# Kernel optimization log

Hardware: AMD Instinct MI355X
Metric: run time of the kernel (lower is better)

The kernel has to match this reference:

```python
import jax, jax.numpy as jnp
import numpy as np
from jax import lax

B, T_Y, T_X = 16, 1600, 400
MEL_C, TXT_C, MAS_C = 80, 512, 384
HID = MAS_C * 2          # SwiGLUConvFFN hidden width (mas_channels*2)
NEG = -1e9


def setup_inputs() -> dict:
    key = jax.random.key(0)
    ks = jax.random.split(key, 20)
    p = lambda k, s: jax.random.normal(k, s, jnp.float32) * 0.02
    return {
        "mel_hidden_states": jax.random.normal(ks[0], (B, T_Y, MEL_C), jnp.float32),
        "text_hidden_states": jax.random.normal(ks[1], (B, T_X, TXT_C), jnp.float32),
        # mel SwiGLU conv-FFN (kernel 5): in->2*HID, gate, HID->MAS_C
        "mel_w1": p(ks[2], (2 * HID, MEL_C, 5)), "mel_b1": jnp.zeros((2 * HID,), jnp.float32),
        "mel_w2": p(ks[3], (MAS_C, HID, 5)),     "mel_b2": jnp.zeros((MAS_C,), jnp.float32),
        # text SwiGLU conv-FFN (kernel 3)
        "txt_w1": p(ks[4], (2 * HID, TXT_C, 3)), "txt_b1": jnp.zeros((2 * HID,), jnp.float32),
        "txt_w2": p(ks[5], (MAS_C, HID, 3)),     "txt_b2": jnp.zeros((MAS_C,), jnp.float32),
        # SimpleAttention query/key projections (value proj does not affect returned outputs)
        "wq": p(ks[6], (MAS_C, MAS_C)), "bq": jnp.zeros((MAS_C,), jnp.float32),
        "wk": p(ks[7], (MAS_C, MAS_C)), "bk": jnp.zeros((MAS_C,), jnp.float32),
        "x_lens": jax.random.randint(ks[8], (B,), T_X // 2, T_X + 1).astype(jnp.int32),
        "y_lens": jax.random.randint(ks[9], (B,), T_Y // 2, T_Y + 1).astype(jnp.int32),
    }


def _conv_ffn(x, pad_mask, w1, b1, w2, b2):
    """SwiGLU/ReGLU conv FFN. x:(B,T,C), pad_mask:(B,T) True=padded."""
    keep = (~pad_mask)[:, None, :].astype(x.dtype)          # (B,1,T)
    h = jnp.transpose(x, (0, 2, 1)) * keep                  # (B,C,T)
    dn = ("NCH", "OIH", "NCH")
    h = lax.conv_general_dilated(h, w1, (1,), "SAME", dimension_numbers=dn) + b1[None, :, None]
    a, g = jnp.split(h, 2, axis=1)
    h = a * jax.nn.relu(g) * keep                           # relugt gating
    h = lax.conv_general_dilated(h, w2, (1,), "SAME", dimension_numbers=dn) + b2[None, :, None]
    return jnp.transpose(h * keep, (0, 2, 1))               # (B,T,out)


def _mas_single(logp, t_x, t_y):
    """Glow-TTS maximum_path for one item. logp:(T_X,T_Y). Returns hard path (T_X,T_Y)."""
    xi = jnp.arange(T_X)
    yi = jnp.arange(T_Y)
    valid = (xi[:, None] < t_x) & (yi[None, :] < t_y) & (xi[:, None] <= yi[None, :])
    lp = jnp.where(valid, logp, NEG)

    def fstep(prev, col):                                   # prev:(T_X,), col:(T_X,)
        shifted = jnp.concatenate([jnp.full((1,), NEG, prev.dtype), prev[:-1]])
        cur = col + jnp.maximum(prev, shifted)
        return cur, cur

    init = jnp.where(xi == 0, 0.0, NEG).astype(logp.dtype)
    _, v = lax.scan(fstep, init, lp.T)                      # v:(T_Y,T_X) DP table

    def bstep(x, y):                                        # backtrack from y=T_Y-1 down
        active = y < t_y
        row = (xi == x) & active
        vp = v[y - 1]
        dec = (x > 0) & ((x == y) | (vp[jnp.maximum(x - 1, 0)] > vp[x]))
        new_x = jnp.where(active & (y > 0) & dec, x - 1, x)
        return new_x, row

    _, rows = lax.scan(bstep, t_x - 1, jnp.arange(T_Y - 1, -1, -1))
    return rows[::-1].T.astype(jnp.float32)                 # (T_X,T_Y)


def _safe_log(t, eps=1e-6):
    return jnp.nan_to_num(jnp.log(t + eps), nan=eps)


def reference(mel_hidden_states, text_hidden_states,
              mel_w1, mel_b1, mel_w2, mel_b2,
              txt_w1, txt_b1, txt_w2, txt_b2,
              wq, bq, wk, bk, x_lens, y_lens):
    x_mask = jnp.arange(T_X)[None, :] >= x_lens[:, None]    # (B,T_X) True=padded
    y_mask = jnp.arange(T_Y)[None, :] >= y_lens[:, None]    # (B,T_Y)

    text_proj = _conv_ffn(text_hidden_states, x_mask, txt_w1, txt_b1, txt_w2, txt_b2)
    mel_proj = _conv_ffn(mel_hidden_states, y_mask, mel_w1, mel_b1, mel_w2, mel_b2)

    q = mel_proj @ wq.T + bq                                # (B,T_Y,D)
    k = text_proj @ wk.T + bk                               # (B,T_X,D)
    scores = jnp.einsum("byd,bxd->byx", q, k) / (MAS_C ** 0.5)
    # expand_masks: mask==0 only where query AND key are both padded (faithful to source)
    both_pad = y_mask[:, :, None] & x_mask[:, None, :]
    scores = jnp.where(both_pad, jnp.float32(-1e-9), scores)
    attn_w = jax.nn.softmax(scores, axis=-1)                # (B,T_Y,T_X)

    avg_attn = attn_w[:, None]                              # (B,1,T_Y,T_X)
    attn_logprob = _safe_log(avg_attn)

    mas_in = jnp.transpose(attn_logprob[:, 0], (0, 2, 1))   # (B,T_X,T_Y)
    attn_hard = lax.stop_gradient(jax.vmap(_mas_single)(mas_in, x_lens, y_lens))
    attn_hard_dur = attn_hard.sum(2)                        # (B,T_X)
    return avg_attn, attn_logprob, attn_hard, attn_hard_dur
```

## Files before the change

kernel.cpp:

```cpp
#include <hip/hip_runtime.h>
#include <cstdint>

#define B 16
#define TY 1600
#define TX 400
#define MAS 384
#define HID 768
#define NEGV -1e9f

typedef __bf16 bf16x8 __attribute__((ext_vector_type(8)));
typedef float  f32x4  __attribute__((ext_vector_type(4)));

__device__ __forceinline__ f32x4 mfma16(bf16x8 a, bf16x8 b, f32x4 c) {
  return __builtin_amdgcn_mfma_f32_16x16x32_bf16(a, b, c, 0, 0, 0);
}

__global__ void split_pad_k(const float* __restrict__ in, __bf16* __restrict__ oh,
                            __bf16* __restrict__ ol, int CIN, int CINP, long n) {
  long i = (long)blockIdx.x * 256 + threadIdx.x;
  if (i >= n) return;
  long row = i / CINP; int ci = (int)(i - row * CINP);
  float v = (ci < CIN) ? in[row * CIN + ci] : 0.f;
  __bf16 h = (__bf16)v;
  oh[i] = h; ol[i] = (__bf16)(v - (float)h);
}

__global__ void wsplit_k(const float* __restrict__ w, __bf16* __restrict__ oh,
                         __bf16* __restrict__ ol, int CIN, int K_, int CINP, long n) {
  long i = (long)blockIdx.x * 256 + threadIdx.x;
  if (i >= n) return;
  long kdspan = (long)K_ * CINP;
  long nn = i / kdspan; int kd = (int)(i - nn * kdspan);
  int k = kd / CINP, ci = kd - k * CINP;
  float v = (ci < CIN) ? w[(nn * CIN + ci) * K_ + k] : 0.f;
  __bf16 h = (__bf16)v;
  oh[i] = h; ol[i] = (__bf16)(v - (float)h);
}

template<int CINP, int K, int T>
__global__ __launch_bounds__(256)
void conv1_mfma(const __bf16* __restrict__ xh, const __bf16* __restrict__ xl,
                const __bf16* __restrict__ wh, const __bf16* __restrict__ wl,
                const float* __restrict__ bias, const int* __restrict__ lens,
                __bf16* __restrict__ hh, __bf16* __restrict__ hl)
{
  constexpr int BM = 128, PAD = K / 2, ROWS = BM + K - 1, KD = K * CINP;
  __shared__ float4 xs[8 * ROWS];
  const int b = blockIdx.z, t0 = blockIdx.x * BM, n0 = blockIdx.y * 64;
  const int tid = threadIdx.x, wid = tid >> 6, lane = tid & 63;
  const int wm = wid >> 1, wn = wid & 1, lr = lane & 15, lg = lane >> 4;
  const int len = lens[b];
  const f32x4 Z4 = {0.f, 0.f, 0.f, 0.f};
  f32x4 acc_a[4][2], acc_g[4][2];
  #pragma unroll
  for (int m = 0; m < 4; ++m)
    #pragma unroll
    for (int n = 0; n < 2; ++n) { acc_a[m][n] = Z4; acc_g[m][n] = Z4; }

  #pragma unroll 1
  for (int ci0 = 0; ci0 < CINP; ci0 += 32) {
    __syncthreads();
    for (int e = tid; e < ROWS * 8; e += 256) {
      int row = e >> 3, sc = e & 7, spl = sc >> 2, cg = sc & 3;
      int t = t0 + row - PAD;
      float4 v = {0.f, 0.f, 0.f, 0.f};
      if (t >= 0 && t < len)
        v = *(const float4*)((spl ? xl : xh) + ((size_t)b * T + t) * CINP + ci0 + cg * 8);
      xs[(spl * 4 + cg) * ROWS + row] = v;
    }
    __syncthreads();
    #pragma unroll
    for (int k = 0; k < K; ++k) {
      bf16x8 ah[4], al[4];
      #pragma unroll
      for (int mf = 0; mf < 4; ++mf) {
        int row = wm * 64 + mf * 16 + lr + k;
        ah[mf] = *(const bf16x8*)&xs[lg * ROWS + row];
        al[mf] = *(const bf16x8*)&xs[(4 + lg) * ROWS + row];
      }
      size_t kd = (size_t)k * CINP + ci0 + lg * 8;
      #pragma unroll
      for (int nf = 0; nf < 2; ++nf) {
        int na = n0 + wn * 32 + nf * 16 + lr;
        bf16x8 bah = *(const bf16x8*)(wh + (size_t)na * KD + kd);
        bf16x8 bal = *(const bf16x8*)(wl + (size_t)na * KD + kd);
        bf16x8 bgh = *(const bf16x8*)(wh + (size_t)(na + HID) * KD + kd);
        bf16x8 bgl = *(const bf16x8*)(wl + (size_t)(na + HID) * KD + kd);
        #pragma unroll
        for (int mf = 0; mf < 4; ++mf) {
          acc_a[mf][nf] = mfma16(ah[mf], bah, acc_a[mf][nf]);
          acc_a[mf][nf] = mfma16(ah[mf], bal, acc_a[mf][nf]);
          acc_a[mf][nf] = mfma16(al[mf], bah, acc_a[mf][nf]);
          acc_g[mf][nf] = mfma16(ah[mf], bgh, acc_g[mf][nf]);
          acc_g[mf][nf] = mfma16(ah[mf], bgl, acc_g[mf][nf]);
          acc_g[mf][nf] = mfma16(al[mf], bgh, acc_g[mf][nf]);
        }
      }
    }
  }
  #pragma unroll
  for (int nf = 0; nf < 2; ++nf) {
    int c = n0 + wn * 32 + nf * 16 + lr;
    float ba = bias[c], bg = bias[c + HID];
    #pragma unroll
    for (int mf = 0; mf < 4; ++mf) {
      #pragma unroll
      for (int r = 0; r < 4; ++r) {
        int t = t0 + wm * 64 + mf * 16 + lg * 4 + r;
        if (t < T) {
          float a = acc_a[mf][nf][r] + ba;
          float g = acc_g[mf][nf][r] + bg;
          float v = a * fmaxf(g, 0.f);
          __bf16 vh = (__bf16)v;
          size_t o = ((size_t)b * T + t) * HID + c;
          hh[o] = vh;
          hl[o] = (__bf16)(v - (float)vh);
        }
      }
    }
  }
}

template<int CINP, int K, int T, bool MASK, bool SPLITOUT, bool STORET>
__global__ __launch_bounds__(256)
void conv2_mfma(const __bf16* __restrict__ xh, const __bf16* __restrict__ xl,
                const __bf16* __restrict__ wh, const __bf16* __restrict__ wl,
                const float* __restrict__ bias, const int* __restrict__ lens,
                float* __restrict__ out, __bf16* __restrict__ oh, __bf16* __restrict__ ol)
{
  constexpr int BM = 64, PAD = K / 2, ROWS = BM + K - 1, STRIDE = ROWS + 1, KD = K * CINP;
  __shared__ float4 xs[8 * STRIDE];
  const int b = blockIdx.z, t0 = blockIdx.x * BM, n0 = blockIdx.y * 128;
  const int tid = threadIdx.x, wn = tid >> 6, lane = tid & 63;
  const int lr = lane & 15, lg = lane >> 4;
  const int len = lens[b];
  const f32x4 Z4 = {0.f, 0.f, 0.f, 0.f};
  f32x4 acc[4][2];
  #pragma unroll
  for (int m = 0; m < 4; ++m)
    #pragma unroll
    for (int n = 0; n < 2; ++n) acc[m][n] = Z4;

  #pragma unroll 1
  for (int ci0 = 0; ci0 < CINP; ci0 += 32) {
    __syncthreads();
    for (int e = tid; e < ROWS * 8; e += 256) {
      int row = e >> 3, sc = e & 7, spl = sc >> 2, cg = sc & 3;
      int t = t0 + row - PAD;
      float4 v = {0.f, 0.f, 0.f, 0.f};
      if (t >= 0 && t < len)
        v = *(const float4*)((spl ? xl : xh) + ((size_t)b * T + t) * CINP + ci0 + cg * 8);
      xs[(spl * 4 + cg) * STRIDE + row] = v;
    }
    __syncthreads();
    #pragma unroll
    for (int k = 0; k < K; ++k) {
      bf16x8 ah[4], al[4];
      #pragma unroll
      for (int mf = 0; mf < 4; ++mf) {
        int row = mf * 16 + lr + k;
        ah[mf] = *(const bf16x8*)&xs[lg * STRIDE + row];
        al[mf] = *(const bf16x8*)&xs[(4 + lg) * STRIDE + row];
      }
      size_t kd = (size_t)k * CINP + ci0 + lg * 8;
      #pragma unroll
      for (int nf = 0; nf < 2; ++nf) {
        int nc = n0 + wn * 32 + nf * 16 + lr;
        bf16x8 bh = *(const bf16x8*)(wh + (size_t)nc * KD + kd);
        bf16x8 bl = *(const bf16x8*)(wl + (size_t)nc * KD + kd);
        #pragma unroll
        for (int mf = 0; mf < 4; ++mf) {
          acc[mf][nf] = mfma16(ah[mf], bh, acc[mf][nf]);
          acc[mf][nf] = mfma16(ah[mf], bl, acc[mf][nf]);
          acc[mf][nf] = mfma16(al[mf], bh, acc[mf][nf]);
        }
      }
    }
  }
  #pragma unroll
  for (int nf = 0; nf < 2; ++nf) {
    int c = n0 + wn * 32 + nf * 16 + lr;
    float bb = bias[c];
    #pragma unroll
    for (int mf = 0; mf < 4; ++mf) {
      #pragma unroll
      for (int r = 0; r < 4; ++r) {
        int t = t0 + mf * 16 + lg * 4 + r;
        if (t < T) {
          float v = acc[mf][nf][r] + bb;
          if (MASK && t >= len) v = 0.f;
          if (SPLITOUT) {
            __bf16 vh = (__bf16)v;
            size_t o = ((size_t)b * T + t) * MAS + c;
            oh[o] = vh;
            ol[o] = (__bf16)(v - (float)vh);
          } else if (STORET) {
            out[((size_t)b * MAS + c) * T + t] = v;
          } else {
            out[((size_t)b * T + t) * MAS + c] = v;
          }
        }
      }
    }
  }
}

__global__ __launch_bounds__(512)
void scores_k(const float* __restrict__ q, const float* __restrict__ kT,
              const int* __restrict__ xl, const int* __restrict__ yl,
              float* __restrict__ oattn, float* __restrict__ ologp)
{
  __shared__ float qs[16 * 384];
  __shared__ float tmp[8];
  const int b = blockIdx.y, y0 = blockIdx.x * 16, tid = threadIdx.x;
  for (int e = tid; e < 16 * 384; e += 512)
    qs[e] = q[((size_t)b * TY + (y0 + e / 384)) * 384 + (e - (e / 384) * 384)];
  __syncthreads();
  float acc[16];
  #pragma unroll
  for (int i = 0; i < 16; ++i) acc[i] = 0.f;
  const int x = tid;
  if (x < TX) {
    const float* kb = kT + (size_t)b * MAS * TX + x;
    for (int d = 0; d < 384; d += 4) {
      float k0 = kb[(size_t)(d + 0) * TX], k1 = kb[(size_t)(d + 1) * TX];
      float k2 = kb[(size_t)(d + 2) * TX], k3 = kb[(size_t)(d + 3) * TX];
      #pragma unroll
      for (int yy = 0; yy < 16; ++yy) {
        float4 qv = *(const float4*)&qs[yy * 384 + d];
        acc[yy] = fmaf(qv.x, k0, fmaf(qv.y, k1, fmaf(qv.z, k2, fmaf(qv.w, k3, acc[yy]))));
      }
    }
  }
  const int xlen = xl[b], ylen = yl[b];
  const float scale = 0.05103103630798288f;
  const bool xpad = (x >= xlen);
  const int wv = tid >> 6, ln = tid & 63;
  #pragma unroll 1
  for (int yy = 0; yy < 16; ++yy) {
    int y = y0 + yy;
    float s = -3.0e38f;
    if (x < TX) {
      s = acc[yy] * scale;
      if (xpad && (y >= ylen)) s = -1e-9f;
    }
    float m = s;
    for (int off = 32; off; off >>= 1) m = fmaxf(m, __shfl_xor(m, off));
    if (ln == 0) tmp[wv] = m;
    __syncthreads();
    float mx = fmaxf(fmaxf(fmaxf(tmp[0], tmp[1]), fmaxf(tmp[2], tmp[3])),
                     fmaxf(fmaxf(tmp[4], tmp[5]), fmaxf(tmp[6], tmp[7])));
    __syncthreads();
    float e = (x < TX) ? expf(s - mx) : 0.f;
    float sm = e;
    for (int off = 32; off; off >>= 1) sm += __shfl_xor(sm, off);
    if (ln == 0) tmp[wv] = sm;
    __syncthreads();
    float tot = tmp[0] + tmp[1] + tmp[2] + tmp[3] + tmp[4] + tmp[5] + tmp[6] + tmp[7];
    __syncthreads();
    if (x < TX) {
      float w = e / tot;
      size_t o = ((size_t)b * TY + y) * TX + x;
      oattn[o] = w;
      ologp[o] = logf(w + 1e-6f);
    }
  }
}

#define MAS_LD(blkv, buf) do {                                           \
    int base_ = (blkv) * 4;                                              \
    _Pragma("unroll")                                                    \
    for (int d_ = 0; d_ < 4; ++d_) {                                     \
      int yr_ = base_ + d_; if (yr_ > TY - 1) yr_ = TY - 1;              \
      const float* r_ = lpb + (size_t)yr_ * TX;                          \
      buf[d_ * 3 + 0] = *(const float4*)(r_ + lb0);                      \
      buf[d_ * 3 + 1] = *(const float4*)(r_ + lb1);                      \
      buf[d_ * 3 + 2] = *(const float4*)(r_ + lb2);                      \
    } } while (0)

#define MAS_BLK(blkv, buf) do {                                          \
    float h0 = __shfl_up(w[8], 1),  h1 = __shfl_up(w[9], 1);             \
    float h2 = __shfl_up(w[10], 1), h3 = __shfl_up(w[11], 1);            \
    w[0] = lane ? h0 : NEGV; w[1] = lane ? h1 : NEGV;                    \
    w[2] = lane ? h2 : NEGV; w[3] = lane ? h3 : NEGV;                    \
    const int y0_ = (blkv) * 4;                                          \
    const bool ph1_ = (y0_ < TX);                                        \
    _Pragma("unroll")                                                    \
    for (int d_ = 0; d_ < 4; ++d_) {                                     \
      const int y_ = y0_ + d_;                                           \
      float lp[12];                                                      \
      _Pragma("unroll")                                                  \
      for (int k_ = 0; k_ < 3; ++k_) {                                   \
        float4 v_ = buf[d_ * 3 + k_];                                    \
        lp[k_*4+0] = v_.x + wxm[k_*4+0]; lp[k_*4+1] = v_.y + wxm[k_*4+1];\
        lp[k_*4+2] = v_.z + wxm[k_*4+2]; lp[k_*4+3] = v_.w + wxm[k_*4+3];\
      }                                                                  \
      if (ph1_) {                                                        \
        int c_ = y_ - p0;                                                \
        _Pragma("unroll")                                                \
        for (int i_ = 0; i_ < 12; ++i_) lp[i_] = (i_ <= c_) ? lp[i_] : NEGV; \
      }                                                                  \
      unsigned byte_ = 0;                                                \
      _Pragma("unroll")                                                  \
      for (int j_ = 0; j_ < 8; ++j_)                                     \
        byte_ |= (w[j_ + 3] > w[j_ + 4]) ? (1u << j_) : 0u;              \
      float nw[12];                                                      \
      nw[0] = lp[0] + w[0];                                              \
      _Pragma("unroll")                                                  \
      for (int i_ = 1; i_ < 12; ++i_) nw[i_] = lp[i_] + fmaxf(w[i_], w[i_ - 1]); \
      bb[(size_t)y_ * 64 + lane] = (unsigned char)byte_;                 \
      _Pragma("unroll")                                                  \
      for (int i_ = 0; i_ < 12; ++i_) w[i_] = nw[i_];                    \
    } } while (0)

__global__ __launch_bounds__(64)
void mas_fwd(const float* __restrict__ logprob, const int* __restrict__ xl,
             const int* __restrict__ yl, unsigned char* __restrict__ bits)
{
  const int b = blockIdx.x;
  const int lane = threadIdx.x;
  const int xlen = xl[b], ylen = yl[b];
  const float* lpb = logprob + (size_t)b * TY * TX;
  unsigned char* bb = bits + (size_t)b * TY * 64;
  const int p0 = lane * 8 - 4;
  int t;
  t = p0;     if (t < 0) t = 0; if (t > 396) t = 396; const int lb0 = t;
  t = p0 + 4; if (t < 0) t = 0; if (t > 396) t = 396; const int lb1 = t;
  t = p0 + 8; if (t < 0) t = 0; if (t > 396) t = 396; const int lb2 = t;

  float w[12], wxm[12];
  #pragma unroll
  for (int i = 0; i < 12; ++i) {
    int p = p0 + i;
    wxm[i] = (p >= 0 && p < xlen) ? 0.f : NEGV;
    w[i] = (p == 0) ? 0.f : NEGV;
  }

  float4 bufA[12], bufB[12];
  MAS_LD(0, bufA);
  MAS_LD(1, bufB);
  const int nblk = (ylen + 3) >> 2;
  int blk = 0;
  #pragma unroll 1
  for (; blk + 1 < nblk; blk += 2) {
    MAS_BLK(blk, bufA);
    MAS_LD(blk + 2, bufA);
    MAS_BLK(blk + 1, bufB);
    MAS_LD(blk + 3, bufB);
  }
  if (blk < nblk) MAS_BLK(blk, bufA);
}

__global__ __launch_bounds__(64)
void mas_bt(const unsigned char* __restrict__ bits, const int* __restrict__ xl,
            const int* __restrict__ yl, float* __restrict__ hard, float* __restrict__ dur)
{
  const int b = blockIdx.x;
  const int lane = threadIdx.x;
  const int xlen = xl[b], ylen = yl[b];
  const unsigned char* bb = bits + (size_t)b * TY * 64;
  float* hb = hard + (size_t)b * TX * TY;
  float* db = dur + (size_t)b * TX;

  int x = xlen - 1;
  int cnt = 0;
  #pragma unroll 1
  for (int ycur = ylen - 1; ycur >= 0; ycur -= 64) {
    int lo = x - 63; if (lo < 0) lo = 0;
    const int wb = (lo >> 3) & ~3;
    int ry = ycur - lane;
    unsigned w0 = 0, w1 = 0, w2 = 0;
    if (ry >= 0) {
      const unsigned* rp = (const unsigned*)(bb + (size_t)ry * 64 + wb);
      w0 = rp[0]; w1 = rp[1]; w2 = rp[2];
    }
    const int rows = (ycur + 1 < 64) ? (ycur + 1) : 64;
    #pragma unroll 1
    for (int s = 0; s < rows; s += 8) {
      const int cnt8 = (rows - s < 8) ? (rows - s) : 8;
      unsigned r0[8], r1[8], r2[8];
      #pragma unroll
      for (int u = 0; u < 8; ++u) {
        r0[u] = (unsigned)__builtin_amdgcn_readlane((int)w0, s + u);
        r1[u] = (unsigned)__builtin_amdgcn_readlane((int)w1, s + u);
        r2[u] = (unsigned)__builtin_amdgcn_readlane((int)w2, s + u);
      }
      #pragma unroll
      for (int u = 0; u < 8; ++u) {
        if (u < cnt8) {
          const int yy = ycur - s - u;
          ++cnt;
          if (yy > 0 && x > 0) {
            const int boff = (x >> 3) - wb;
            const unsigned word = (boff < 4) ? r0[u] : ((boff < 8) ? r1[u] : r2[u]);
            const unsigned byte = word >> ((boff & 3) * 8);
            if ((x == yy) || ((byte >> (x & 7)) & 1)) {
              for (int q = lane; q < cnt; q += 64) hb[(size_t)x * TY + yy + q] = 1.0f;
              if (lane == 0) db[x] = (float)cnt;
              cnt = 0;
              --x;
            }
          }
        }
      }
    }
  }
  for (int q = lane; q < cnt; q += 64) hb[(size_t)x * TY + q] = 1.0f;
  if (lane == 0) db[x] = (float)cnt;
}

extern "C" void kernel_launch(void* const* d_in, const int* in_sizes, int n_in,
                              void* d_out, int out_size, void* d_ws, size_t ws_size,
                              hipStream_t stream) {
  const float* mel_x  = (const float*)d_in[0];
  const float* txt_x  = (const float*)d_in[1];
  const float* mel_w1 = (const float*)d_in[2];
  const float* mel_b1 = (const float*)d_in[3];
  const float* mel_w2 = (const float*)d_in[4];
  const float* mel_b2 = (const float*)d_in[5];
  const float* txt_w1 = (const float*)d_in[6];
  const float* txt_b1 = (const float*)d_in[7];
  const float* txt_w2 = (const float*)d_in[8];
  const float* txt_b2 = (const float*)d_in[9];
  const float* wq     = (const float*)d_in[10];
  const float* bq     = (const float*)d_in[11];
  const float* wk     = (const float*)d_in[12];
  const float* bk     = (const float*)d_in[13];
  const int*   xl     = (const int*)d_in[14];
  const int*   yl     = (const int*)d_in[15];

  char* wsb = (char*)d_ws;
  constexpr size_t MXH  = 0;
  constexpr size_t MXL  = MXH  + 4915200;
  constexpr size_t TXH  = MXL  + 4915200;
  constexpr size_t TXL  = TXH  + 6553600;
  constexpr size_t TPH  = TXH;
  constexpr size_t TPL  = TXH  + 4915200;
  constexpr size_t W1MH = TXL  + 6553600;
  constexpr size_t W1ML = W1MH + 1474560;
  constexpr size_t W2MH = W1ML + 1474560;
  constexpr size_t W2ML = W2MH + 2949120;
  constexpr size_t W1TH = W2ML + 2949120;
  constexpr size_t W1TL = W1TH + 4718592;
  constexpr size_t W2TH = W1TL + 4718592;
  constexpr size_t W2TL = W2TH + 1769472;
  constexpr size_t WQH  = W2TL + 1769472;
  constexpr size_t WQL  = WQH  + 294912;
  constexpr size_t WKH  = WQL  + 294912;
  constexpr size_t WKL  = WKH  + 294912;
  constexpr size_t HH   = WKL  + 294912;
  constexpr size_t HL   = HH   + 39321600;
  constexpr size_t QB   = HH;
  constexpr size_t KTB  = HL;
  constexpr size_t BITS = HL   + 10240000;
  constexpr size_t PH   = HL   + 39321600;
  constexpr size_t PL   = PH   + 19660800;

  float* out = (float*)d_out;
  float* o_attn = out;
  float* o_logp = out + (size_t)10240000;
  float* o_hard = out + (size_t)20480000;
  float* o_dur  = out + (size_t)30720000;

  hipMemsetAsync(o_hard, 0, (size_t)(10240000 + 6400) * sizeof(float), stream);

  split_pad_k<<<9600, 256, 0, stream>>>(mel_x, (__bf16*)(wsb + MXH), (__bf16*)(wsb + MXL), 80, 96, 2457600L);
  split_pad_k<<<12800, 256, 0, stream>>>(txt_x, (__bf16*)(wsb + TXH), (__bf16*)(wsb + TXL), 512, 512, 3276800L);
  wsplit_k<<<2880, 256, 0, stream>>>(mel_w1, (__bf16*)(wsb + W1MH), (__bf16*)(wsb + W1ML), 80, 5, 96, 737280L);
  wsplit_k<<<5760, 256, 0, stream>>>(mel_w2, (__bf16*)(wsb + W2MH), (__bf16*)(wsb + W2ML), 768, 5, 768, 1474560L);
  wsplit_k<<<9216, 256, 0, stream>>>(txt_w1, (__bf16*)(wsb + W1TH), (__bf16*)(wsb + W1TL), 512, 3, 512, 2359296L);
  wsplit_k<<<3456, 256, 0, stream>>>(txt_w2, (__bf16*)(wsb + W2TH), (__bf16*)(wsb + W2TL), 768, 3, 768, 884736L);
  wsplit_k<<<576, 256, 0, stream>>>(wq, (__bf16*)(wsb + WQH), (__bf16*)(wsb + WQL), 384, 1, 384, 147456L);
  wsplit_k<<<576, 256, 0, stream>>>(wk, (__bf16*)(wsb + WKH), (__bf16*)(wsb + WKL), 384, 1, 384, 147456L);

  conv1_mfma<512, 3, 400><<<dim3(4, 12, B), 256, 0, stream>>>(
      (const __bf16*)(wsb + TXH), (const __bf16*)(wsb + TXL),
      (const __bf16*)(wsb + W1TH), (const __bf16*)(wsb + W1TL),
      txt_b1, xl, (__bf16*)(wsb + HH), (__bf16*)(wsb + HL));
  conv2_mfma<768, 3, 400, true, true, false><<<dim3(7, 3, B), 256, 0, stream>>>(
      (const __bf16*)(wsb + HH), (const __bf16*)(wsb + HL),
      (const __bf16*)(wsb + W2TH), (const __bf16*)(wsb + W2TL),
      txt_b2, xl, nullptr, (__bf16*)(wsb + TPH), (__bf16*)(wsb + TPL));

  conv1_mfma<96, 5, 1600><<<dim3(13, 12, B), 256, 0, stream>>>(
      (const __bf16*)(wsb + MXH), (const __bf16*)(wsb + MXL),
      (const __bf16*)(wsb + W1MH), (const __bf16*)(wsb + W1ML),
      mel_b1, yl, (__bf16*)(wsb + HH), (__bf16*)(wsb + HL));
  conv2_mfma<768, 5, 1600, true, true, false><<<dim3(25, 3, B), 256, 0, stream>>>(
      (const __bf16*)(wsb + HH), (const __bf16*)(wsb + HL),
      (const __bf16*)(wsb + W2MH), (const __bf16*)(wsb + W2ML),
      mel_b2, yl, nullptr, (__bf16*)(wsb + PH), (__bf16*)(wsb + PL));

  conv2_mfma<384, 1, 400, false, false, true><<<dim3(7, 3, B), 256, 0, stream>>>(
      (const __bf16*)(wsb + TPH), (const __bf16*)(wsb + TPL),
      (const __bf16*)(wsb + WKH), (const __bf16*)(wsb + WKL),
      bk, xl, (float*)(wsb + KTB), nullptr, nullptr);
  conv2_mfma<384, 1, 1600, false, false, false><<<dim3(25, 3, B), 256, 0, stream>>>(
      (const __bf16*)(wsb + PH), (const __bf16*)(wsb + PL),
      (const __bf16*)(wsb + WQH), (const __bf16*)(wsb + WQL),
      bq, yl, (float*)(wsb + QB), nullptr, nullptr);

  scores_k<<<dim3(100, B), 512, 0, stream>>>(
      (const float*)(wsb + QB), (const float*)(wsb + KTB), xl, yl, o_attn, o_logp);
  mas_fwd<<<B, 64, 0, stream>>>(o_logp, xl, yl, (unsigned char*)(wsb + BITS));
  mas_bt<<<B, 64, 0, stream>>>((const unsigned char*)(wsb + BITS), xl, yl, o_hard, o_dur);
}
```

Baseline: 1.639 ms.

## Fold Q/K projections into second conv weights and retile conv2

The Q and K linear projections are folded into the second conv-FFN convolution weights by precomputing Wq·W2 and Wk·W2 with an MFMA kernel, and the projected conv2 biases are folded into per-channel constants. This removes two projection GEMM launches and the bf16 split intermediate outputs of conv2. conv2 is also retiled to 512 threads covering 192 output channels per block. The fold adds a small per-call weight GEMM and changes rounding of the folded weights, though the hi/lo split keeps precision.

New measurement: 2.025 ms. 1.24x slower.

```diff
diff --git a/kernel.cpp b/kernel.cpp
--- a/kernel.cpp
+++ b/kernel.cpp
@@ -35,6 +35,90 @@
   float v = (ci < CIN) ? w[(nn * CIN + ci) * K_ + k] : 0.f;
   __bf16 h = (__bf16)v;
   oh[i] = h; ol[i] = (__bf16)(v - (float)h);
+}
+
+__global__ void tsplit_k(const float* __restrict__ in, __bf16* __restrict__ oh,
+                         __bf16* __restrict__ ol, int JTOT, long n) {
+  long i = (long)blockIdx.x * 256 + threadIdx.x;
+  if (i >= n) return;
+  int m = (int)(i / JTOT), j = (int)(i - (long)m * JTOT);
+  float v = in[i];
+  long o = (long)j * 384 + m;
+  __bf16 h = (__bf16)v;
+  oh[o] = h; ol[o] = (__bf16)(v - (float)h);
+}
+
+__global__ void fold_bias_k(const float* __restrict__ wq, const float* __restrict__ b,
+                            float* __restrict__ o) {
+  int n = threadIdx.x;
+  float s = 0.f;
+  for (int m = 0; m < 384; ++m) s = fmaf(wq[n * 384 + m], b[m], s);
+  o[n] = s;
+}
+
+template<int KK>
+__global__ __launch_bounds__(256)
+void fold_mfma(const __bf16* __restrict__ xh, const __bf16* __restrict__ xl,
+               const __bf16* __restrict__ wh, const __bf16* __restrict__ wl,
+               __bf16* __restrict__ oh, __bf16* __restrict__ ol)
+{
+  constexpr int CINP = 384, ROWS = 64, STRIDE = 65;
+  __shared__ float4 xs[8 * STRIDE];
+  const int t0 = blockIdx.x * 64, n0 = blockIdx.y * 128;
+  const int tid = threadIdx.x, wn = tid >> 6, lane = tid & 63;
+  const int lr = lane & 15, lg = lane >> 4;
+  const f32x4 Z4 = {0.f, 0.f, 0.f, 0.f};
+  f32x4 acc[4][2];
+  #pragma unroll
+  for (int m = 0; m < 4; ++m) { acc[m][0] = Z4; acc[m][1] = Z4; }
+
+  #pragma unroll 1
+  for (int ci0 = 0; ci0 < CINP; ci0 += 32) {
+    __syncthreads();
+    for (int e = tid; e < ROWS * 8; e += 256) {
+      int row = e >> 3, sc = e & 7, spl = sc >> 2, cg = sc & 3;
+      int t = t0 + row;
+      xs[(spl * 4 + cg) * STRIDE + row] =
+          *(const float4*)((spl ? xl : xh) + (size_t)t * CINP + ci0 + cg * 8);
+    }
+    __syncthreads();
+    bf16x8 ah[4], al[4];
+    #pragma unroll
+    for (int mf = 0; mf < 4; ++mf) {
+      int row = mf * 16 + lr;
+      ah[mf] = *(const bf16x8*)&xs[lg * STRIDE + row];
+      al[mf] = *(const bf16x8*)&xs[(4 + lg) * STRIDE + row];
+    }
+    size_t kd = (size_t)ci0 + lg * 8;
+    #pragma unroll
+    for (int nf = 0; nf < 2; ++nf) {
+      int nc = n0 + wn * 32 + nf * 16 + lr;
+      bf16x8 bh = *(const bf16x8*)(wh + (size_t)nc * 384 + kd);
+      bf16x8 bl = *(const bf16x8*)(wl + (size_t)nc * 384 + kd);
+      #pragma unroll
+      for (int mf = 0; mf < 4; ++mf) {
+        acc[mf][nf] = mfma16(ah[mf], bh, acc[mf][nf]);
+        acc[mf][nf] = mfma16(ah[mf], bl, acc[mf][nf]);
+        acc[mf][nf] = mfma16(al[mf], bh, acc[mf][nf]);
+      }
+    }
+  }
+  #pragma unroll
+  for (int nf = 0; nf < 2; ++nf) {
+    int c = n0 + wn * 32 + nf * 16 + lr;
+    #pragma unroll
+    for (int mf = 0; mf < 4; ++mf) {
+      #pragma unroll
+      for (int r = 0; r < 4; ++r) {
+        int j = t0 + mf * 16 + lg * 4 + r;
+        int k = j % KK, ci = j / KK;
+        size_t o = (size_t)c * (KK * HID) + (size_t)k * HID + ci;
+        float v = acc[mf][nf][r];
+        __bf16 vh = (__bf16)v;
+        oh[o] = vh; ol[o] = (__bf16)(v - (float)vh);
+      }
+    }
+  }
 }
 
 template<int CINP, int K, int T>
@@ -121,30 +205,30 @@
   }
 }
 
-template<int CINP, int K, int T, bool MASK, bool SPLITOUT, bool STORET>
-__global__ __launch_bounds__(256)
+template<int CINP, int K, int T, bool STORET>
+__global__ __launch_bounds__(512)
 void conv2_mfma(const __bf16* __restrict__ xh, const __bf16* __restrict__ xl,
                 const __bf16* __restrict__ wh, const __bf16* __restrict__ wl,
-                const float* __restrict__ bias, const int* __restrict__ lens,
-                float* __restrict__ out, __bf16* __restrict__ oh, __bf16* __restrict__ ol)
+                const float* __restrict__ bias, const float* __restrict__ ab,
+                const int* __restrict__ lens, float* __restrict__ out)
 {
   constexpr int BM = 64, PAD = K / 2, ROWS = BM + K - 1, STRIDE = ROWS + 1, KD = K * CINP;
   __shared__ float4 xs[8 * STRIDE];
-  const int b = blockIdx.z, t0 = blockIdx.x * BM, n0 = blockIdx.y * 128;
-  const int tid = threadIdx.x, wn = tid >> 6, lane = tid & 63;
-  const int lr = lane & 15, lg = lane >> 4;
+  const int b = blockIdx.z, t0 = blockIdx.x * BM, n0 = blockIdx.y * 192;
+  const int tid = threadIdx.x, wid = tid >> 6, lane = tid & 63;
+  const int wm = wid >> 2, wn = wid & 3, lr = lane & 15, lg = lane >> 4;
   const int len = lens[b];
   const f32x4 Z4 = {0.f, 0.f, 0.f, 0.f};
-  f32x4 acc[4][2];
-  #pragma unroll
-  for (int m = 0; m < 4; ++m)
-    #pragma unroll
-    for (int n = 0; n < 2; ++n) acc[m][n] = Z4;
+  f32x4 acc[2][3];
+  #pragma unroll
+  for (int m = 0; m < 2; ++m)
+    #pragma unroll
+    for (int n = 0; n < 3; ++n) acc[m][n] = Z4;
 
   #pragma unroll 1
   for (int ci0 = 0; ci0 < CINP; ci0 += 32) {
     __syncthreads();
-    for (int e = tid; e < ROWS * 8; e += 256) {
+    for (int e = tid; e < ROWS * 8; e += 512) {
       int row = e >> 3, sc = e & 7, spl = sc >> 2, cg = sc & 3;
       int t = t0 + row - PAD;
       float4 v = {0.f, 0.f, 0.f, 0.f};
@@ -155,21 +239,21 @@
     __syncthreads();
     #pragma unroll
     for (int k = 0; k < K; ++k) {
-      bf16x8 ah[4], al[4];
-      #pragma unroll
-      for (int mf = 0; mf < 4; ++mf) {
-        int row = mf * 16 + lr + k;
+      bf16x8 ah[2], al[2];
+      #pragma unroll
+      for (int mf = 0; mf < 2; ++mf) {
+        int row = wm * 32 + mf * 16 + lr + k;
         ah[mf] = *(const bf16x8*)&xs[lg * STRIDE + row];
         al[mf] = *(const bf16x8*)&xs[(4 + lg) * STRIDE + row];
       }
       size_t kd = (size_t)k * CINP + ci0 + lg * 8;
       #pragma unroll
-      for (int nf = 0; nf < 2; ++nf) {
-        int nc = n0 + wn * 32 + nf * 16 + lr;
+      for (int nf = 0; nf < 3; ++nf) {
+        int nc = n0 + wn * 48 + nf * 16 + lr;
         bf16x8 bh = *(const bf16x8*)(wh + (size_t)nc * KD + kd);
         bf16x8 bl = *(const bf16x8*)(wl + (size_t)nc * KD + kd);
         #pragma unroll
-        for (int mf = 0; mf < 4; ++mf) {
+        for (int mf = 0; mf < 2; ++mf) {
           acc[mf][nf] = mfma16(ah[mf], bh, acc[mf][nf]);
           acc[mf][nf] = mfma16(ah[mf], bl, acc[mf][nf]);
           acc[mf][nf] = mfma16(al[mf], bh, acc[mf][nf]);
@@ -178,27 +262,20 @@
     }
   }
   #pragma unroll
-  for (int nf = 0; nf < 2; ++nf) {
-    int c = n0 + wn * 32 + nf * 16 + lr;
-    float bb = bias[c];
-    #pragma unroll
-    for (int mf = 0; mf < 4; ++mf) {
+  for (int nf = 0; nf < 3; ++nf) {
+    int c = n0 + wn * 48 + nf * 16 + lr;
+    float bb = bias[c], aB = ab[c];
+    #pragma unroll
+    for (int mf = 0; mf < 2; ++mf) {
       #pragma unroll
       for (int r = 0; r < 4; ++r) {
-        int t = t0 + mf * 16 + lg * 4 + r;
+        int t = t0 + wm * 32 + mf * 16 + lg * 4 + r;
         if (t < T) {
           float v = acc[mf][nf][r] + bb;
-          if (MASK && t >= len) v = 0.f;
-          if (SPLITOUT) {
-            __bf16 vh = (__bf16)v;
-            size_t o = ((size_t)b * T + t) * MAS + c;
-            oh[o] = vh;
-            ol[o] = (__bf16)(v - (float)vh);
-          } else if (STORET) {
-            out[((size_t)b * MAS + c) * T + t] = v;
-          } else {
-            out[((size_t)b * T + t) * MAS + c] = v;
-          }
+          if (t >= len) v = 0.f;
+          v += aB;
+          if (STORET) out[((size_t)b * MAS + c) * T + t] = v;
+          else        out[((size_t)b * T + t) * MAS + c] = v;
         }
       }
     }
@@ -430,31 +507,34 @@
   const int*   yl     = (const int*)d_in[15];
 
   char* wsb = (char*)d_ws;
-  constexpr size_t MXH  = 0;
-  constexpr size_t MXL  = MXH  + 4915200;
-  constexpr size_t TXH  = MXL  + 4915200;
-  constexpr size_t TXL  = TXH  + 6553600;
-  constexpr size_t TPH  = TXH;
-  constexpr size_t TPL  = TXH  + 4915200;
-  constexpr size_t W1MH = TXL  + 6553600;
-  constexpr size_t W1ML = W1MH + 1474560;
-  constexpr size_t W2MH = W1ML + 1474560;
-  constexpr size_t W2ML = W2MH + 2949120;
-  constexpr size_t W1TH = W2ML + 2949120;
-  constexpr size_t W1TL = W1TH + 4718592;
-  constexpr size_t W2TH = W1TL + 4718592;
-  constexpr size_t W2TL = W2TH + 1769472;
-  constexpr size_t WQH  = W2TL + 1769472;
-  constexpr size_t WQL  = WQH  + 294912;
-  constexpr size_t WKH  = WQL  + 294912;
-  constexpr size_t WKL  = WKH  + 294912;
-  constexpr size_t HH   = WKL  + 294912;
-  constexpr size_t HL   = HH   + 39321600;
-  constexpr size_t QB   = HH;
-  constexpr size_t KTB  = HL;
-  constexpr size_t BITS = HL   + 10240000;
-  constexpr size_t PH   = HL   + 39321600;
-  constexpr size_t PL   = PH   + 19660800;
+  constexpr size_t MXH   = 0;
+  constexpr size_t MXL   = MXH   + 4915200;
+  constexpr size_t TXH   = MXL   + 4915200;
+  constexpr size_t TXL   = TXH   + 6553600;
+  constexpr size_t KTF   = TXH;
+  constexpr size_t WFMH  = TXL   + 6553600;
+  constexpr size_t WFML  = WFMH  + 2949120;
+  constexpr size_t WFTH  = WFML  + 2949120;
+  constexpr size_t WFTL  = WFTH  + 1769472;
+  constexpr size_t B2M   = WFTL  + 1769472;
+  constexpr size_t B2T   = B2M   + 2048;
+  constexpr size_t HH    = B2T   + 2048;
+  constexpr size_t HL    = HH    + 39321600;
+  constexpr size_t BITS  = MXH;
+  constexpr size_t SCR   = HL    + 39321600;
+  constexpr size_t W1MH  = SCR;
+  constexpr size_t W1ML  = W1MH  + 1474560;
+  constexpr size_t W1TH  = W1ML  + 1474560;
+  constexpr size_t W1TL  = W1TH  + 4718592;
+  constexpr size_t WQH   = W1TL  + 4718592;
+  constexpr size_t WQL   = WQH   + 294912;
+  constexpr size_t WKH   = WQL   + 294912;
+  constexpr size_t WKL   = WKH   + 294912;
+  constexpr size_t W2TMH = WKL   + 294912;
+  constexpr size_t W2TML = W2TMH + 2949120;
+  constexpr size_t W2TTH = W2TML + 2949120;
+  constexpr size_t W2TTL = W2TTH + 1769472;
+  constexpr size_t QF    = SCR;
 
   float* out = (float*)d_out;
   float* o_attn = out;
@@ -467,41 +547,42 @@
   split_pad_k<<<9600, 256, 0, stream>>>(mel_x, (__bf16*)(wsb + MXH), (__bf16*)(wsb + MXL), 80, 96, 2457600L);
   split_pad_k<<<12800, 256, 0, stream>>>(txt_x, (__bf16*)(wsb + TXH), (__bf16*)(wsb + TXL), 512, 512, 3276800L);
   wsplit_k<<<2880, 256, 0, stream>>>(mel_w1, (__bf16*)(wsb + W1MH), (__bf16*)(wsb + W1ML), 80, 5, 96, 737280L);
-  wsplit_k<<<5760, 256, 0, stream>>>(mel_w2, (__bf16*)(wsb + W2MH), (__bf16*)(wsb + W2ML), 768, 5, 768, 1474560L);
   wsplit_k<<<9216, 256, 0, stream>>>(txt_w1, (__bf16*)(wsb + W1TH), (__bf16*)(wsb + W1TL), 512, 3, 512, 2359296L);
-  wsplit_k<<<3456, 256, 0, stream>>>(txt_w2, (__bf16*)(wsb + W2TH), (__bf16*)(wsb + W2TL), 768, 3, 768, 884736L);
   wsplit_k<<<576, 256, 0, stream>>>(wq, (__bf16*)(wsb + WQH), (__bf16*)(wsb + WQL), 384, 1, 384, 147456L);
   wsplit_k<<<576, 256, 0, stream>>>(wk, (__bf16*)(wsb + WKH), (__bf16*)(wsb + WKL), 384, 1, 384, 147456L);
+  tsplit_k<<<5760, 256, 0, stream>>>(mel_w2, (__bf16*)(wsb + W2TMH), (__bf16*)(wsb + W2TML), 3840, 1474560L);
+  tsplit_k<<<3456, 256, 0, stream>>>(txt_w2, (__bf16*)(wsb + W2TTH), (__bf16*)(wsb + W2TTL), 2304, 884736L);
+  fold_mfma<5><<<dim3(60, 3), 256, 0, stream>>>(
+      (const __bf16*)(wsb + W2TMH), (const __bf16*)(wsb + W2TML),
+      (const __bf16*)(wsb + WQH), (const __bf16*)(wsb + WQL),
+      (__bf16*)(wsb + WFMH), (__bf16*)(wsb + WFML));
+  fold_mfma<3><<<dim3(36, 3), 256, 0, stream>>>(
+      (const __bf16*)(wsb + W2TTH), (const __bf16*)(wsb + W2TTL),
+      (const __bf16*)(wsb + WKH), (const __bf16*)(wsb + WKL),
+      (__bf16*)(wsb + WFTH), (__bf16*)(wsb + WFTL));
+  fold_bias_k<<<1, 384, 0, stream>>>(wq, mel_b2, (float*)(wsb + B2M));
+  fold_bias_k<<<1, 384, 0, stream>>>(wk, txt_b2, (float*)(wsb + B2T));
 
   conv1_mfma<512, 3, 400><<<dim3(4, 12, B), 256, 0, stream>>>(
       (const __bf16*)(wsb + TXH), (const __bf16*)(wsb + TXL),
       (const __bf16*)(wsb + W1TH), (const __bf16*)(wsb + W1TL),
       txt_b1, xl, (__bf16*)(wsb + HH), (__bf16*)(wsb + HL));
-  conv2_mfma<768, 3, 400, true, true, false><<<dim3(7, 3, B), 256, 0, stream>>>(
+  conv2_mfma<768, 3, 400, true><<<dim3(7, 2, B), 512, 0, stream>>>(
       (const __bf16*)(wsb + HH), (const __bf16*)(wsb + HL),
-      (const __bf16*)(wsb + W2TH), (const __bf16*)(wsb + W2TL),
-      txt_b2, xl, nullptr, (__bf16*)(wsb + TPH), (__bf16*)(wsb + TPL));
+      (const __bf16*)(wsb + WFTH), (const __bf16*)(wsb + WFTL),
+      (const float*)(wsb + B2T), bk, xl, (float*)(wsb + KTF));
 
   conv1_mfma<96, 5, 1600><<<dim3(13, 12, B), 256, 0, stream>>>(
       (const __bf16*)(wsb + MXH), (const __bf16*)(wsb + MXL),
       (const __bf16*)(wsb + W1MH), (const __bf16*)(wsb + W1ML),
       mel_b1, yl, (__bf16*)(wsb + HH), (__bf16*)(wsb + HL));
-  conv2_mfma<768, 5, 1600, true, true, false><<<dim3(25, 3, B), 256, 0, stream>>>(
+  conv2_mfma<768, 5, 1600, false><<<dim3(25, 2, B), 512, 0, stream>>>(
       (const __bf16*)(wsb + HH), (const __bf16*)(wsb + HL),
-      (const __bf16*)(wsb + W2MH), (const __bf16*)(wsb + W2ML),
-      mel_b2, yl, nullptr, (__bf16*)(wsb + PH), (__bf16*)(wsb + PL));
-
-  conv2_mfma<384, 1, 400, false, false, true><<<dim3(7, 3, B), 256, 0, stream>>>(
-      (const __bf16*)(wsb + TPH), (const __bf16*)(wsb + TPL),
-      (const __bf16*)(wsb + WKH), (const __bf16*)(wsb + WKL),
-      bk, xl, (float*)(wsb + KTB), nullptr, nullptr);
-  conv2_mfma<384, 1, 1600, false, false, false><<<dim3(25, 3, B), 256, 0, stream>>>(
-      (const __bf16*)(wsb + PH), (const __bf16*)(wsb + PL),
-      (const __bf16*)(wsb + WQH), (const __bf16*)(wsb + WQL),
-      bq, yl, (float*)(wsb + QB), nullptr, nullptr);
+      (const __bf16*)(wsb + WFMH), (const __bf16*)(wsb + WFML),
+      (const float*)(wsb + B2M), bq, yl, (float*)(wsb + QF));
 
   scores_k<<<dim3(100, B), 512, 0, stream>>>(
-      (const float*)(wsb + QB), (const float*)(wsb + KTB), xl, yl, o_attn, o_logp);
+      (const float*)(wsb + QF), (const float*)(wsb + KTF), xl, yl, o_attn, o_logp);
   mas_fwd<<<B, 64, 0, stream>>>(o_logp, xl, yl, (unsigned char*)(wsb + BITS));
   mas_bt<<<B, 64, 0, stream>>>((const unsigned char*)(wsb + BITS), xl, yl, o_hard, o_dur);
 }
```
